# Performance work log

Hardware: AMD Instinct MI355X
Metric: run time of the kernel (lower is better)

## Reference

```python
import jax, jax.numpy as jnp
import numpy as np
from jax.scipy.special import logsumexp

B, S, K = 512, 2048, 17

def setup_inputs() -> dict:
    key = jax.random.key(0)
    k_em, k_lab, k_len, k_st, k_en, k_tr = jax.random.split(key, 6)
    emissions = jax.random.normal(k_em, (B, S, K), dtype=jnp.float32)
    labels = jax.random.randint(k_lab, (B, S), 0, K, dtype=jnp.int64).astype(jnp.int32)
    # ragged valid-prefix mask; torchcrf requires mask[:, 0] to be all True
    lengths = jax.random.randint(k_len, (B,), 1, S + 1)
    attention_mask = (jnp.arange(S)[None, :] < lengths[:, None]).astype(jnp.int32)
    # CRF params (torchcrf inits uniform(-0.1, 0.1))
    start_transitions = jax.random.uniform(k_st, (K,), minval=-0.1, maxval=0.1, dtype=jnp.float32)
    end_transitions = jax.random.uniform(k_en, (K,), minval=-0.1, maxval=0.1, dtype=jnp.float32)
    transitions = jax.random.uniform(k_tr, (K, K), minval=-0.1, maxval=0.1, dtype=jnp.float32)
    return {
        "emissions": emissions,
        "start_transitions": start_transitions,
        "end_transitions": end_transitions,
        "transitions": transitions,
        "labels": labels,
        "attention_mask": attention_mask,
    }


def _crf_neg_log_likelihood(emissions, start_transitions, end_transitions, transitions,
                            labels, mask_bool):
    # emissions: [B,S,K], labels: [B,S] int, mask_bool: [B,S] bool (mask[:,0] all True)
    mask_f = mask_bool.astype(emissions.dtype)
    b_idx = jnp.arange(emissions.shape[0])

    # ---- numerator: score of the gold path ----
    first_tags = labels[:, 0]                                  # [B]
    num = start_transitions[first_tags] + emissions[b_idx, 0, first_tags]
    prev_tags = labels[:, :-1]                                 # [B,S-1]
    cur_tags = labels[:, 1:]                                   # [B,S-1]
    emit_t = jnp.take_along_axis(emissions[:, 1:, :], cur_tags[..., None], axis=-1)[..., 0]
    step_scores = transitions[prev_tags, cur_tags] + emit_t    # [B,S-1]
    num = num + jnp.sum(step_scores * mask_f[:, 1:], axis=1)
    seq_ends = jnp.sum(mask_bool, axis=1).astype(jnp.int32) - 1  # [B]
    last_tags = jnp.take_along_axis(labels, seq_ends[:, None], axis=1)[:, 0]
    num = num + end_transitions[last_tags]

    # ---- denominator: log partition via forward algorithm (lax.scan over time) ----
    alpha0 = start_transitions[None, :] + emissions[:, 0, :]   # [B,K]

    def step(alpha, xs):
        emit, m = xs                                           # emit [B,K], m [B] bool
        # alpha[b, i] + transitions[i, j] + emit[b, j] -> logsumexp over i
        nxt = logsumexp(alpha[:, :, None] + transitions[None, :, :] + emit[:, None, :], axis=1)
        alpha = jnp.where(m[:, None], nxt, alpha)
        return alpha, None

    em_seq = jnp.swapaxes(emissions[:, 1:, :], 0, 1)           # [S-1,B,K]
    m_seq = jnp.swapaxes(mask_bool[:, 1:], 0, 1)               # [S-1,B]
    alpha, _ = jax.lax.scan(step, alpha0, (em_seq, m_seq))
    log_z = logsumexp(alpha + end_transitions[None, :], axis=1)  # [B]

    llh = num - log_z
    return -jnp.mean(llh)  # torchcrf reduction='mean', loss = -crf(...)


def reference(emissions, start_transitions, end_transitions, transitions, labels, attention_mask):
    mask_bool = attention_mask.astype(bool) & (labels >= 0)
    labels_c = jnp.where(labels == -100, 0, labels)
    loss = _crf_neg_log_likelihood(emissions, start_transitions, end_transitions,
                                   transitions, labels_c, mask_bool)
    return loss, emissions
```

## Files before the change

kernel.cpp:

```cpp
#include <hip/hip_runtime.h>
#include <cstddef>

#define NB 512
#define NS 2048
#define NK 17
#define CL 8
#define NW 4
#define HT 1024
#define SP 8
#define NLT (HT + SP)
#define CHUNKD 37
#define ROWD 9
#define LDS_DW ((NLT / 4) * CHUNKD)

typedef __fp16 h2 __attribute__((ext_vector_type(2)));
typedef float  f4 __attribute__((ext_vector_type(4)));
union UH { unsigned int u; h2 h; };

__global__ void prep_k(const float* __restrict__ trans, const int* __restrict__ attn,
                       unsigned int* __restrict__ Mg, int* __restrict__ lens) {
    __shared__ int red[4];
    const int tid = threadIdx.x;
    if (blockIdx.x == 0) {
        if (tid < 9 * NK) {
            int kk = tid / NK, n = tid % NK;
            float lo = __expf(trans[(2 * kk) * NK + n]);
            float hi = (kk < 8) ? __expf(trans[(2 * kk + 1) * NK + n]) : 0.f;
            UH u; u.h = __builtin_amdgcn_cvt_pkrtz(lo, hi);
            Mg[tid] = u.u;
        }
        return;
    }
    const int b = blockIdx.x - 1;
    const int4* __restrict__ a4 = (const int4*)(attn + (size_t)b * NS);
    int4 x = a4[tid];
    int4 y = a4[tid + 256];
    int s = x.x + x.y + x.z + x.w + y.x + y.y + y.z + y.w;
#pragma unroll
    for (int off = 32; off >= 1; off >>= 1) s += __shfl_down(s, off, 64);
    if ((tid & 63) == 0) red[tid >> 6] = s;
    __syncthreads();
    if (tid == 0) lens[b] = red[0] + red[1] + red[2] + red[3];
}

__global__ __launch_bounds__(256, 4) void crf_fused(
    const float* __restrict__ emis,
    const float* __restrict__ startT,
    const float* __restrict__ endT,
    const float* __restrict__ trans,
    const int*   __restrict__ labels,
    const int*   __restrict__ lens,
    const unsigned int* __restrict__ Mg,
    float*       __restrict__ outE,
    float*       __restrict__ out)
{
    __shared__ unsigned int expE[LDS_DW];
    float* red = (float*)expE;

    const int tid = threadIdx.x;
    const int b  = blockIdx.x >> 1;
    const int h  = blockIdx.x & 1;
    const int T0 = h << 10;
    const int len = lens[b];

    const size_t ebOff = (size_t)b * NS * NK;
    const float* __restrict__ eb = emis + ebOff;
    float*       __restrict__ ob = outE + ebOff;
    const int*   __restrict__ lb = labels + (size_t)b * NS;

    const int endF = (T0 + HT) * NK;
    const int ownF = T0 * NK;

    if (T0 >= len) {
        const float* __restrict__ src = eb + ownF;
        float*       __restrict__ dst = ob + ownF;
        const int base = tid * 4;
        f4 r0 = *(const f4*)(src + base);
        f4 r1 = *(const f4*)(src + base + 1024);
        f4 r2 = *(const f4*)(src + base + 2048);
        f4 r3 = *(const f4*)(src + base + 3072);
#pragma unroll
        for (int k = 0; k < 3; ++k) {
            const int o = k * 4096 + base;
            f4 n0 = *(const f4*)(src + o + 4096);
            f4 n1 = *(const f4*)(src + o + 5120);
            f4 n2 = *(const f4*)(src + o + 6144);
            f4 n3 = *(const f4*)(src + o + 7168);
            __builtin_nontemporal_store(r0, (f4*)(dst + o));
            __builtin_nontemporal_store(r1, (f4*)(dst + o + 1024));
            __builtin_nontemporal_store(r2, (f4*)(dst + o + 2048));
            __builtin_nontemporal_store(r3, (f4*)(dst + o + 3072));
            r0 = n0; r1 = n1; r2 = n2; r3 = n3;
        }
        const int o = 12288 + base;
        f4 n0 = *(const f4*)(src + o + 4096);
        __builtin_nontemporal_store(r0, (f4*)(dst + o));
        __builtin_nontemporal_store(r1, (f4*)(dst + o + 1024));
        __builtin_nontemporal_store(r2, (f4*)(dst + o + 2048));
        __builtin_nontemporal_store(r3, (f4*)(dst + o + 3072));
        __builtin_nontemporal_store(n0, (f4*)(dst + o + 4096));
        return;
    }

    const int loadT0 = (h == 0) ? 0 : (T0 - SP);
    const int baseF  = loadT0 * NK;
    const int lenF   = len * NK;

    {
        int g = baseF + tid * 4;
        int t4  = (int)((unsigned)g / 17u);
        int n4  = g - t4 * 17;
        int lt4 = t4 - (T0 - SP);
        const f4 z = {0.f, 0.f, 0.f, 0.f};
        f4 r0 = (g          < endF) ? *(const f4*)(eb + g         ) : z;
        f4 r1 = (g + 1024   < endF) ? *(const f4*)(eb + g + 1024  ) : z;
        f4 r2 = (g + 2048   < endF) ? *(const f4*)(eb + g + 2048  ) : z;
        f4 r3 = (g + 3072   < endF) ? *(const f4*)(eb + g + 3072  ) : z;
        while (g < endF) {
            f4 nx = (g + 4096 < endF) ? *(const f4*)(eb + g + 4096) : z;
            if (g >= ownF) __builtin_nontemporal_store(r0, (f4*)(ob + g));
            if (g < lenF) {
                float ev[4] = {r0.x, r0.y, r0.z, r0.w};
                int lt = lt4, nn = n4;
#pragma unroll
                for (int u = 0; u < 4; ++u) {
                    int ha = ((lt >> 2) * CHUNKD + (lt & 3) * ROWD) * 2 + nn;
                    ((__fp16*)expE)[ha] = (__fp16)__expf(ev[u]);
                    ++nn; if (nn == 17) { nn = 0; ++lt; }
                }
            }
            lt4 += 60; n4 += 4; if (n4 >= 17) { n4 -= 17; ++lt4; }
            r0 = r1; r1 = r2; r2 = r3; r3 = nx;
            g += 1024;
        }
    }
    __syncthreads();

    float numA = 0.f, zc = 0.f;

    if (tid >= 128) {
        int t = T0 + (tid - 128);
#pragma unroll
        for (int j = 0; j < 8; ++j, t += 128) {
            if (t < len) {
                int la = lb[t];
                numA += eb[(size_t)t * NK + la];
                numA += (t == 0) ? startT[la] : trans[lb[t - 1] * NK + la];
                if (t == len - 1) numA += endT[la];
            }
        }
    } else if (T0 + ((tid & 64) << 3) < len) {
        const int gc = h * 128 + tid;
        const int t0 = gc * CL;
        const int cE = (len - 1) >> 3;
        float logscale = 0.f, endlog = 0.f;
        bool hasEnd = false;
        h2 wh[9];
        {
            const __fp16 iv = (__fp16)(1.f / NK);
#pragma unroll
            for (int kk = 0; kk < 9; ++kk) { wh[kk].x = iv; wh[kk].y = iv; }
            wh[8].y = (__fp16)0.f;
        }

        if (gc == 0) {
            float wf[NK]; float ssum = 0.f;
            const int bdw = (SP >> 2) * CHUNKD;
#pragma unroll
            for (int k = 0; k < 9; ++k) {
                UH u; u.u = expE[bdw + k];
                int n = 2 * k;
                wf[n] = __expf(startT[n]) * (float)u.h.x;
                if (n + 1 < NK) wf[n + 1] = __expf(startT[n + 1]) * (float)u.h.y;
            }
#pragma unroll
            for (int n = 0; n < NK; ++n) ssum += wf[n];
            float r = 1.f / ssum;
            logscale = __logf(ssum);
#pragma unroll
            for (int kk = 0; kk < 8; ++kk)
                wh[kk] = __builtin_amdgcn_cvt_pkrtz(wf[2 * kk] * r, wf[2 * kk + 1] * r);
            wh[8] = __builtin_amdgcn_cvt_pkrtz(wf[16] * r, 0.f);
            if (len == 1) {
                float sd = 0.f;
#pragma unroll
                for (int n = 0; n < NK; ++n) sd += wf[n] * __expf(endT[n]);
                endlog = __logf(sd);
                hasEnd = true;
            }
        }

#pragma unroll 1
        for (int i = 0; i < CL + NW; ++i) {
            int t = t0 - NW + i;
            bool active = (t >= 1);
            int ta = active ? t : 1;
            int lt = ta - (T0 - SP);
            int bdw = (lt >> 2) * CHUNKD + (lt & 3) * ROWD;
            float ex[NK + 1];
#pragma unroll
            for (int k = 0; k < 9; ++k) {
                UH u; u.u = expE[bdw + k];
                ex[2 * k]     = (float)u.h.x;
                ex[2 * k + 1] = (float)u.h.y;
            }
            if (gc != 0 && t == t0) logscale = 0.f;

            float acc[NK];
#pragma unroll
            for (int n = 0; n < NK; ++n) acc[n] = 0.f;
#pragma unroll
            for (int kk = 0; kk < 9; ++kk) {
                h2 w = wh[kk];
#pragma unroll
                for (int n = 0; n < NK; ++n) {
                    UH u; u.u = Mg[kk * NK + n];
                    acc[n] = __builtin_amdgcn_fdot2(w, u.h, acc[n], false);
                }
            }
            float wf[NK]; float ssum = 0.f;
#pragma unroll
            for (int n = 0; n < NK; ++n) {
                float w = acc[n] * ex[n];
                wf[n] = w;
                ssum += w;
            }
            float r  = __builtin_amdgcn_rcpf(ssum);
            float lg = __logf(ssum);
            if (active) {
                if (t >= t0 && t == len - 1) {
                    float sd = 0.f;
#pragma unroll
                    for (int n = 0; n < NK; ++n) sd += wf[n] * __expf(endT[n]);
                    endlog = logscale + __logf(sd);
                    hasEnd = true;
                }
                logscale += lg;
#pragma unroll
                for (int kk = 0; kk < 8; ++kk)
                    wh[kk] = __builtin_amdgcn_cvt_pkrtz(wf[2 * kk] * r, wf[2 * kk + 1] * r);
                wh[8] = __builtin_amdgcn_cvt_pkrtz(wf[16] * r, 0.f);
            }
        }

        zc = ((gc < cE) ? logscale : 0.f) + (hasEnd ? endlog : 0.f);
    }

    __syncthreads();
    red[tid] = numA - zc;
    __syncthreads();
    for (int k = 128; k >= 1; k >>= 1) { if (tid < k) red[tid] += red[tid + k]; __syncthreads(); }
    if (tid == 0) atomicAdd(out, -red[0] * (1.f / (float)NB));
}

extern "C" void kernel_launch(void* const* d_in, const int* in_sizes, int n_in,
                              void* d_out, int out_size, void* d_ws, size_t ws_size,
                              hipStream_t stream) {
    (void)in_sizes; (void)n_in; (void)out_size; (void)ws_size;
    const float* emis   = (const float*)d_in[0];
    const float* startT = (const float*)d_in[1];
    const float* endT   = (const float*)d_in[2];
    const float* trans  = (const float*)d_in[3];
    const int*   labels = (const int*)d_in[4];
    const int*   attn   = (const int*)d_in[5];
    float* out = (float*)d_out;
    unsigned int* Mg = (unsigned int*)d_ws;
    int* lens        = (int*)((char*)d_ws + 1024);

    (void)hipMemsetAsync(d_out, 0, sizeof(float), stream);
    prep_k<<<NB + 1, 256, 0, stream>>>(trans, attn, Mg, lens);
    crf_fused<<<NB * 2, 256, 0, stream>>>(emis, startT, endT, trans, labels,
                                          lens, Mg, out + 1, out);
}
```

Measured before the change: 169.6 us.

## Split emissions passthrough copy into dedicated blocks separate from CRF compute

The grid is doubled. The extra 1024 blocks each copy one 1024-timestep slab of emissions to the output with nontemporal stores. The compute blocks no longer write the copy and load only up to the valid sequence length rather than the whole half, so padded timesteps are not read. This spreads the memory-bound copy across more blocks and shortens the critical path of the serial forward recurrence blocks. In exchange, compute blocks now read emissions that copy blocks also read (extra traffic), and the prefetch depth in the load loop drops from four to one.

```diff
diff --git a/kernel.cpp b/kernel.cpp
--- a/kernel.cpp
+++ b/kernel.cpp
@@ -12,6 +12,7 @@
 #define CHUNKD 37
 #define ROWD 9
 #define LDS_DW ((NLT / 4) * CHUNKD)
+#define SLABF (HT * NK)
 
 typedef __fp16 h2 __attribute__((ext_vector_type(2)));
 typedef float  f4 __attribute__((ext_vector_type(4)));
@@ -58,22 +59,11 @@
     float* red = (float*)expE;
 
     const int tid = threadIdx.x;
-    const int b  = blockIdx.x >> 1;
-    const int h  = blockIdx.x & 1;
-    const int T0 = h << 10;
-    const int len = lens[b];
-
-    const size_t ebOff = (size_t)b * NS * NK;
-    const float* __restrict__ eb = emis + ebOff;
-    float*       __restrict__ ob = outE + ebOff;
-    const int*   __restrict__ lb = labels + (size_t)b * NS;
-
-    const int endF = (T0 + HT) * NK;
-    const int ownF = T0 * NK;
-
-    if (T0 >= len) {
-        const float* __restrict__ src = eb + ownF;
-        float*       __restrict__ dst = ob + ownF;
+
+    if (blockIdx.x >= NB * 2) {
+        const size_t off = (size_t)(blockIdx.x - NB * 2) * SLABF;
+        const float* __restrict__ src = emis + off;
+        float*       __restrict__ dst = outE + off;
         const int base = tid * 4;
         f4 r0 = *(const f4*)(src + base);
         f4 r1 = *(const f4*)(src + base + 1024);
@@ -102,36 +92,43 @@
         return;
     }
 
-    const int loadT0 = (h == 0) ? 0 : (T0 - SP);
-    const int baseF  = loadT0 * NK;
-    const int lenF   = len * NK;
+    const int b  = blockIdx.x >> 1;
+    const int h  = blockIdx.x & 1;
+    const int T0 = h << 10;
+    const int len = lens[b];
+
+    if (T0 >= len) return;
+
+    const size_t ebOff = (size_t)b * NS * NK;
+    const float* __restrict__ eb = emis + ebOff;
+    const int*   __restrict__ lb = labels + (size_t)b * NS;
 
     {
-        int g = baseF + tid * 4;
+        const int startF = ((h == 0) ? 0 : (T0 - SP)) * NK;
+        const int Tstop  = (len < T0 + HT) ? len : (T0 + HT);
+        const int stopF  = Tstop * NK;
+        int g = startF + tid * 4;
         int t4  = (int)((unsigned)g / 17u);
         int n4  = g - t4 * 17;
         int lt4 = t4 - (T0 - SP);
-        const f4 z = {0.f, 0.f, 0.f, 0.f};
-        f4 r0 = (g          < endF) ? *(const f4*)(eb + g         ) : z;
-        f4 r1 = (g + 1024   < endF) ? *(const f4*)(eb + g + 1024  ) : z;
-        f4 r2 = (g + 2048   < endF) ? *(const f4*)(eb + g + 2048  ) : z;
-        f4 r3 = (g + 3072   < endF) ? *(const f4*)(eb + g + 3072  ) : z;
-        while (g < endF) {
-            f4 nx = (g + 4096 < endF) ? *(const f4*)(eb + g + 4096) : z;
-            if (g >= ownF) __builtin_nontemporal_store(r0, (f4*)(ob + g));
-            if (g < lenF) {
-                float ev[4] = {r0.x, r0.y, r0.z, r0.w};
-                int lt = lt4, nn = n4;
-#pragma unroll
-                for (int u = 0; u < 4; ++u) {
+        f4 v = {0.f, 0.f, 0.f, 0.f};
+        if (g < stopF) v = *(const f4*)(eb + g);
+        while (g < stopF) {
+            const int gn = g + 1024;
+            f4 vn = v;
+            if (gn < stopF) vn = *(const f4*)(eb + gn);
+            float ev[4] = {v.x, v.y, v.z, v.w};
+            int lt = lt4, nn = n4;
+#pragma unroll
+            for (int u = 0; u < 4; ++u) {
+                if (g + u < stopF) {
                     int ha = ((lt >> 2) * CHUNKD + (lt & 3) * ROWD) * 2 + nn;
                     ((__fp16*)expE)[ha] = (__fp16)__expf(ev[u]);
-                    ++nn; if (nn == 17) { nn = 0; ++lt; }
                 }
+                ++nn; if (nn == 17) { nn = 0; ++lt; }
             }
             lt4 += 60; n4 += 4; if (n4 >= 17) { n4 -= 17; ++lt4; }
-            r0 = r1; r1 = r2; r2 = r3; r3 = nx;
-            g += 1024;
+            v = vn; g = gn;
         }
     }
     __syncthreads();
@@ -269,6 +266,6 @@
 
     (void)hipMemsetAsync(d_out, 0, sizeof(float), stream);
     prep_k<<<NB + 1, 256, 0, stream>>>(trans, attn, Mg, lens);
-    crf_fused<<<NB * 2, 256, 0, stream>>>(emis, startT, endT, trans, labels,
+    crf_fused<<<NB * 4, 256, 0, stream>>>(emis, startT, endT, trans, labels,
                                           lens, Mg, out + 1, out);
 }
```

Result: faster. 156.6 us (-7.6%).
